# Optimization experiments

Measured on AMD Instinct MI355X. Metric: run time of the kernel, lower is better.

Reference implementation:

```python
import jax, jax.numpy as jnp
from jax import lax
import numpy as np

H, V, B, L, T = 512, 64, 32, 2048, 32


def setup_inputs() -> dict:
    key = jax.random.key(0)
    ks = jax.random.split(key, 24)
    s = 0.05
    n = lambda k, shp: jax.random.normal(k, shp, dtype=jnp.float32) * s
    return {
        "init_decoder_input": jax.random.randint(ks[0], (B,), 0, V),
        "h0": n(ks[1], (1, B, H)),
        "c0": n(ks[2], (1, B, H)),
        "encoder_outputs": jax.random.normal(ks[3], (L, B, H), dtype=jnp.float32),
        "labels": jax.random.randint(ks[4], (T, B), 0, V),
        "mask": jnp.ones((T, B), dtype=bool),
        "target_length": T,
        "embed": n(ks[5], (V, H)),
        "W_ih": n(ks[6], (4 * H, H)),
        "W_hh": n(ks[7], (4 * H, H)),
        "b_ih": n(ks[8], (4 * H,)),
        "b_hh": n(ks[9], (4 * H,)),
        "W_concat": n(ks[10], (H, 2 * H)),
        "b_concat": n(ks[11], (H,)),
        "W_out": n(ks[12], (V, H)),
        "b_out": n(ks[13], (V,)),
        "conv_w": n(ks[14], (H, 1, 3)),
        "conv_b": n(ks[15], (H,)),
        "Wq": n(ks[16], (H, H)),
        "Wv": n(ks[17], (H, H)),
        "Ws": n(ks[18], (1, H)),
        "bs": n(ks[19], (1,)),
        "attn_bias": jax.random.uniform(ks[20], (H,), minval=-0.1, maxval=0.1, dtype=jnp.float32),
    }


def reference(init_decoder_input, h0, c0, encoder_outputs, labels, mask, target_length,
              embed, W_ih, W_hh, b_ih, b_hh, W_concat, b_concat, W_out, b_out,
              conv_w, conv_b, Wq, Wv, Ws, bs, attn_bias):
    value = jnp.transpose(encoder_outputs, (1, 0, 2))        # (B, L, H)
    v_proj = value @ Wv.T                                    # value_proj is step-invariant: hoist out of loop
    bsz = value.shape[0]

    def step(carry, xs):
        h, c, last_attn, dec_in, loss = carry
        lab, msk = xs
        # --- embedding + LSTM cell (torch gate order i,f,g,o) ---
        emb = embed[dec_in]                                  # (B, H)
        gates = emb @ W_ih.T + b_ih + h @ W_hh.T + b_hh
        i, f, g, o = jnp.split(gates, 4, axis=-1)
        c_new = jax.nn.sigmoid(f) * c + jax.nn.sigmoid(i) * jnp.tanh(g)
        h_new = jax.nn.sigmoid(o) * jnp.tanh(c_new)
        # --- location-aware attention ---
        conv_attn = lax.conv_general_dilated(
            last_attn[:, None, :], conv_w, (1,), [(1, 1)],
            dimension_numbers=("NCH", "OIH", "NCH"))         # (B, H, L)
        conv_attn = jnp.transpose(conv_attn, (0, 2, 1)) + conv_b  # (B, L, H)
        q = (h_new @ Wq.T)[:, None, :]                       # (B, 1, H)
        score = jnp.squeeze(jnp.tanh(q + v_proj + conv_attn + attn_bias) @ Ws.T, -1) + bs[0]  # (B, L)
        score = jax.nn.sigmoid(score)                        # smoothing=True
        attn = score / jnp.sum(score, axis=-1, keepdims=True)
        context = jnp.einsum("bl,blh->bh", attn, value)
        # --- concat + output ---
        concat_out = jnp.tanh(jnp.concatenate([h_new, context], axis=-1) @ W_concat.T + b_concat)
        logits = concat_out @ W_out.T + b_out                # (B, V)
        probs = jax.nn.softmax(logits, axis=-1)
        pred = jnp.argmax(probs, axis=-1)                    # greedy feedback (detached)
        # --- masked NLL on softmax probs ---
        ce = -jnp.log(probs[jnp.arange(bsz), lab])
        m = msk.astype(probs.dtype)
        step_loss = jnp.sum(ce * m) / jnp.maximum(jnp.sum(m), 1.0)
        step_loss = jnp.where(jnp.any(msk), step_loss, jnp.zeros((), probs.dtype))
        return (h_new, c_new, attn, pred, loss + step_loss), pred

    carry0 = (h0[0], c0[0], jnp.zeros((bsz, value.shape[1]), value.dtype),
              init_decoder_input, jnp.zeros((), jnp.float32))
    (_, _, _, _, loss), preds = lax.scan(step, carry0, (labels, mask))
    return loss, preds.T                                     # (B, T)
```

## Files before the change

### kernel.cpp

```cpp
#include <hip/hip_runtime.h>
#include <math.h>


#define Hdim 512
#define Vdim 64
#define Bdim 32
#define Ldim 2048
#define Tdim 32
#define CLEN 32
#define NCH 64

__device__ __forceinline__ float sigmoid_f(float x) {
  return 1.0f / (1.0f + __expf(-x));
}
__device__ __forceinline__ float tanh_f(float x) {
  float ax = fabsf(x);
  float e = __expf(2.0f * ax);
  float r = 1.0f - 2.0f / (e + 1.0f);
  return copysignf(r, x);
}

__global__ void k_init(const int* __restrict__ init_in, const float* __restrict__ h0,
                       const float* __restrict__ c0, float* __restrict__ h,
                       float* __restrict__ c, float* __restrict__ Sprev,
                       float* __restrict__ ssum, int* __restrict__ curin,
                       float* __restrict__ lossb) {
  int i = blockIdx.x * blockDim.x + threadIdx.x;
  if (i < Bdim * Hdim) { h[i] = h0[i]; c[i] = c0[i]; }
  if (i < Bdim * Ldim) Sprev[i] = 0.0f;
  if (i < Bdim) { ssum[32 + i] = 1.0f; curin[i] = init_in[i]; }
  if (i == 0) lossb[0] = 0.0f;
}

__global__ void k_pack(const float* __restrict__ conv_w, const float* __restrict__ conv_b,
                       const float* __restrict__ attn_bias, const float* __restrict__ Ws,
                       float4* __restrict__ P4, float* __restrict__ cbab) {
  int h = blockIdx.x * blockDim.x + threadIdx.x;
  if (h < Hdim) {
    P4[h] = make_float4(conv_w[3 * h], conv_w[3 * h + 1], conv_w[3 * h + 2], Ws[h]);
    cbab[h] = conv_b[h] + attn_bias[h];
  }
}

__global__ void k_transpose(const float* __restrict__ in, float* __restrict__ out,
                            int R, int C) {
  int i = blockIdx.x * blockDim.x + threadIdx.x;
  if (i < R * C) { int r = i / C, c = i % C; out[(size_t)c * R + r] = in[i]; }
}

__global__ __launch_bounds__(256) void k_matT16(
    const float* __restrict__ A, const float* __restrict__ W,
    float* __restrict__ out, int Kdim, int Ntot, int mode,
    const int* __restrict__ curin, const float* __restrict__ ex1,
    const float* __restrict__ ex2) {
  __shared__ float a_lds[64][33];
  __shared__ float w_lds[64][17];
  const int tid = threadIdx.x;
  const int n0 = blockIdx.x * 16;
  const int m0 = blockIdx.y * 32;
  const int tm = tid >> 3;
  const int tn = tid & 7;
  float acc0 = 0.f, acc1 = 0.f;
  for (int k0 = 0; k0 < Kdim; k0 += 64) {
    {
      const int m = tid & 31, kg = tid >> 5;
      const float* ap = A + (size_t)(m0 + m) * Kdim + k0 + kg * 8;
      float4 v0 = *(const float4*)ap;
      float4 v1 = *(const float4*)(ap + 4);
      const int kk = kg * 8;
      a_lds[kk + 0][m] = v0.x; a_lds[kk + 1][m] = v0.y;
      a_lds[kk + 2][m] = v0.z; a_lds[kk + 3][m] = v0.w;
      a_lds[kk + 4][m] = v1.x; a_lds[kk + 5][m] = v1.y;
      a_lds[kk + 6][m] = v1.z; a_lds[kk + 7][m] = v1.w;
    }
    if (tid < 128) {
      const int r = tid & 15, kg = tid >> 4;
      const float* wp = W + (size_t)(n0 + r) * Kdim + k0 + kg * 8;
      float4 v0 = *(const float4*)wp;
      float4 v1 = *(const float4*)(wp + 4);
      const int kk = kg * 8;
      w_lds[kk + 0][r] = v0.x; w_lds[kk + 1][r] = v0.y;
      w_lds[kk + 2][r] = v0.z; w_lds[kk + 3][r] = v0.w;
      w_lds[kk + 4][r] = v1.x; w_lds[kk + 5][r] = v1.y;
      w_lds[kk + 6][r] = v1.z; w_lds[kk + 7][r] = v1.w;
    }
    __syncthreads();
#pragma unroll 16
    for (int kk = 0; kk < 64; kk++) {
      const float a = a_lds[kk][tm];
      acc0 += a * w_lds[kk][tn * 2];
      acc1 += a * w_lds[kk][tn * 2 + 1];
    }
    __syncthreads();
  }
  const int gm = m0 + tm;
#pragma unroll
  for (int c = 0; c < 2; c++) {
    const int n = n0 + tn * 2 + c;
    const float a = (c == 0) ? acc0 : acc1;
    float r;
    if (mode == 0)      r = a + ex1[(size_t)curin[gm] * 2048 + n];
    else if (mode == 1) r = a + ex1[n];
    else if (mode == 2) r = a + ex1[n] + ex2[n];
    else                r = tanh_f(a + ex1[n]);
    out[(size_t)gm * Ntot + n] = r;
  }
}

__global__ __launch_bounds__(256) void k_vproj(const float* __restrict__ enc,
                                               const float* __restrict__ Wv,
                                               float* __restrict__ vp) {
  __shared__ float At[8][128];
  __shared__ float Bt[8][128];
  const int tid = threadIdx.x;
  const int r0 = blockIdx.x * 128;
  const int c0 = blockIdx.y * 128;
  const int tx = tid & 15;
  const int ty = tid >> 4;
  float acc[8][8];
#pragma unroll
  for (int i = 0; i < 8; i++)
#pragma unroll
    for (int j = 0; j < 8; j++) acc[i][j] = 0.f;

  for (int k0 = 0; k0 < Hdim; k0 += 8) {
    {
      const int r = tid & 127;
      const int kg = tid >> 7;
      const int gr = r0 + r;
      const int b = gr >> 11;
      const int l = gr & (Ldim - 1);
      const float* ap = enc + ((size_t)l * Bdim + b) * Hdim + k0 + kg * 4;
      float4 v = *(const float4*)ap;
      At[kg * 4 + 0][r] = v.x; At[kg * 4 + 1][r] = v.y;
      At[kg * 4 + 2][r] = v.z; At[kg * 4 + 3][r] = v.w;
      const float* wp = Wv + (size_t)(c0 + r) * Hdim + k0 + kg * 4;
      float4 w = *(const float4*)wp;
      Bt[kg * 4 + 0][r] = w.x; Bt[kg * 4 + 1][r] = w.y;
      Bt[kg * 4 + 2][r] = w.z; Bt[kg * 4 + 3][r] = w.w;
    }
    __syncthreads();
#pragma unroll
    for (int kk = 0; kk < 8; kk++) {
      float a[8], bb[8];
      *(float4*)&a[0] = *(const float4*)&At[kk][ty * 8];
      *(float4*)&a[4] = *(const float4*)&At[kk][ty * 8 + 4];
      *(float4*)&bb[0] = *(const float4*)&Bt[kk][tx * 4];
      *(float4*)&bb[4] = *(const float4*)&Bt[kk][64 + tx * 4];
#pragma unroll
      for (int i = 0; i < 8; i++)
#pragma unroll
        for (int j = 0; j < 8; j++) acc[i][j] += a[i] * bb[j];
    }
    __syncthreads();
  }
#pragma unroll
  for (int i = 0; i < 8; i++) {
    float* orow = vp + (size_t)(r0 + ty * 8 + i) * Hdim + c0;
    float4 o0 = {acc[i][0], acc[i][1], acc[i][2], acc[i][3]};
    float4 o1 = {acc[i][4], acc[i][5], acc[i][6], acc[i][7]};
    *(float4*)(orow + tx * 4) = o0;
    *(float4*)(orow + 64 + tx * 4) = o1;
  }
}

__global__ void k_cell(const float* __restrict__ gates, float* __restrict__ h,
                       float* __restrict__ c, float* __restrict__ ssum_cur) {
  int i = blockIdx.x * blockDim.x + threadIdx.x;
  if (blockIdx.x == 0 && threadIdx.x < Bdim) ssum_cur[threadIdx.x] = 0.f;
  int b = i >> 9, hh = i & 511;
  const float* g = gates + (size_t)b * 2048;
  float gi = g[hh], gf = g[512 + hh], gg = g[1024 + hh], go = g[1536 + hh];
  float cn = sigmoid_f(gf) * c[i] + sigmoid_f(gi) * tanh_f(gg);
  float hn = sigmoid_f(go) * tanh_f(cn);
  c[i] = cn;
  h[i] = hn;
}

__global__ __launch_bounds__(256) void k_sctx(
    const float* __restrict__ vp, const float* __restrict__ q2,
    const float* __restrict__ Sprev, const float* __restrict__ ssum_prev,
    const float4* __restrict__ P4, const float* __restrict__ bs,
    const float* __restrict__ enc, float* __restrict__ Scur,
    float* __restrict__ ssum_cur, float* __restrict__ pctx) {
  __shared__ float pad[4][512];
  __shared__ float wsum[4];
  const int chunk = blockIdx.x & (NCH - 1);
  const int b = blockIdx.x >> 6;
  const int tid = threadIdx.x;
  const int wave = tid >> 6, lane = tid & 63;
  const int l0 = chunk * CLEN + wave * 8;

  float4 pp[8];
#pragma unroll
  for (int e = 0; e < 8; e++) pp[e] = P4[lane * 8 + e];
  float qv[8];
  {
    const float* qrow = q2 + (size_t)b * Hdim + lane * 8;
    *(float4*)&qv[0] = *(const float4*)qrow;
    *(float4*)&qv[4] = *(const float4*)(qrow + 4);
  }
  const float inv = 1.0f / ssum_prev[b];
  const float* sp = Sprev + (size_t)b * Ldim;
  const float bsv = bs[0];

  float acc[8];
#pragma unroll
  for (int e = 0; e < 8; e++) acc[e] = 0.f;
  float csum = 0.f;

#pragma unroll 2
  for (int i = 0; i < 8; i++) {
    const int l = l0 + i;
    const float* vrow = vp + ((size_t)b * Ldim + l) * Hdim + lane * 8;
    const float* erow = enc + ((size_t)l * Bdim + b) * Hdim + lane * 8;
    float vv[8];
    *(float4*)&vv[0] = *(const float4*)vrow;
    *(float4*)&vv[4] = *(const float4*)(vrow + 4);
    const float4 e0 = *(const float4*)erow;
    const float4 e1 = *(const float4*)(erow + 4);
    const float a0 = (l > 0) ? sp[l - 1] * inv : 0.f;
    const float a1 = sp[l] * inv;
    const float a2 = (l < Ldim - 1) ? sp[l + 1] * inv : 0.f;
    float s = 0.f;
#pragma unroll
    for (int e = 0; e < 8; e++) {
      float x = vv[e] + qv[e] + pp[e].x * a0 + pp[e].y * a1 + pp[e].z * a2;
      s += pp[e].w * tanh_f(x);
    }
#pragma unroll
    for (int off = 32; off; off >>= 1) s += __shfl_xor(s, off, 64);
    const float sg = 1.0f / (1.0f + __expf(-(s + bsv)));
    csum += sg;
    if (lane == 0) Scur[(size_t)b * Ldim + l] = sg;
    acc[0] += sg * e0.x; acc[1] += sg * e0.y;
    acc[2] += sg * e0.z; acc[3] += sg * e0.w;
    acc[4] += sg * e1.x; acc[5] += sg * e1.y;
    acc[6] += sg * e1.z; acc[7] += sg * e1.w;
  }
  *(float4*)&pad[wave][lane * 8] = *(float4*)&acc[0];
  *(float4*)&pad[wave][lane * 8 + 4] = *(float4*)&acc[4];
  if (lane == 0) wsum[wave] = csum;
  __syncthreads();
  float* o = pctx + ((size_t)b * NCH + chunk) * Hdim;
  o[tid] = pad[0][tid] + pad[1][tid] + pad[2][tid] + pad[3][tid];
  o[tid + 256] = pad[0][tid + 256] + pad[1][tid + 256] + pad[2][tid + 256] + pad[3][tid + 256];
  if (tid == 0) atomicAdd(ssum_cur + b, wsum[0] + wsum[1] + wsum[2] + wsum[3]);
}

__global__ __launch_bounds__(256) void k_hcat(
    const float* __restrict__ h, const float* __restrict__ pctx,
    const float* __restrict__ ssum, float* __restrict__ hcat) {
  __shared__ float4 red[256];
  const int b = blockIdx.x;
  const int tid = threadIdx.x;
  const float inv = 1.0f / ssum[b];
  const float4* p4 = (const float4*)(pctx + (size_t)b * NCH * Hdim);
  const int q = tid & 127, ch0 = tid >> 7;
  float4 a = {0.f, 0.f, 0.f, 0.f};
  for (int ch = ch0; ch < NCH; ch += 2) {
    float4 v = p4[ch * 128 + q];
    a.x += v.x; a.y += v.y; a.z += v.z; a.w += v.w;
  }
  red[tid] = a;
  hcat[(size_t)b * 1024 + tid] = h[(size_t)b * Hdim + tid];
  hcat[(size_t)b * 1024 + tid + 256] = h[(size_t)b * Hdim + tid + 256];
  __syncthreads();
  if (tid < 128) {
    float4 r0 = red[tid], r1 = red[tid + 128];
    float4 c4 = {(r0.x + r1.x) * inv, (r0.y + r1.y) * inv,
                 (r0.z + r1.z) * inv, (r0.w + r1.w) * inv};
    *(float4*)&hcat[(size_t)b * 1024 + 512 + q * 4] = c4;
  }
}

__global__ __launch_bounds__(256) void k_out2(
    const float* __restrict__ co, const float* __restrict__ WoT,
    const float* __restrict__ b_out, const int* __restrict__ labels, int t,
    int* __restrict__ curin, float* __restrict__ lossb, float* __restrict__ d_out) {
  __shared__ float cs[512];
  const int b = blockIdx.x;
  const int tid = threadIdx.x;
  cs[tid] = co[(size_t)b * Hdim + tid];
  cs[tid + 256] = co[(size_t)b * Hdim + tid + 256];
  __syncthreads();
  if (tid < 64) {
    float l0 = 0.f, l1 = 0.f, l2 = 0.f, l3 = 0.f;
    for (int k = 0; k < 512; k += 4) {
      l0 += cs[k] * WoT[(size_t)k * 64 + tid];
      l1 += cs[k + 1] * WoT[(size_t)(k + 1) * 64 + tid];
      l2 += cs[k + 2] * WoT[(size_t)(k + 2) * 64 + tid];
      l3 += cs[k + 3] * WoT[(size_t)(k + 3) * 64 + tid];
    }
    const float lg = ((l0 + l1) + (l2 + l3)) + b_out[tid];
    float mx = lg;
    int mi = tid;
#pragma unroll
    for (int off = 32; off; off >>= 1) {
      float ov = __shfl_xor(mx, off, 64);
      int oi = __shfl_xor(mi, off, 64);
      if (ov > mx || (ov == mx && oi < mi)) { mx = ov; mi = oi; }
    }
    float se = __expf(lg - mx);
#pragma unroll
    for (int off = 32; off; off >>= 1) se += __shfl_xor(se, off, 64);
    const int lab = labels[t * Bdim + b];
    const float lg_lab = __shfl(lg, lab, 64);
    if (tid == 0) {
      const float ce = -(lg_lab - mx - __logf(se));
      atomicAdd(lossb, ce * (1.0f / 32.0f));
      curin[b] = mi;
      d_out[1 + b * Tdim + t] = (float)mi;
    }
  }
}

__global__ void k_final(const float* __restrict__ lossb, float* __restrict__ d_out) {
  if (threadIdx.x == 0) d_out[0] = lossb[0];
}

extern "C" void kernel_launch(void* const* d_in, const int* in_sizes, int n_in,
                              void* d_out, int out_size, void* d_ws, size_t ws_size,
                              hipStream_t stream) {
  const int* init_in = (const int*)d_in[0];
  const float* h0 = (const float*)d_in[1];
  const float* c0 = (const float*)d_in[2];
  const float* enc = (const float*)d_in[3];
  const int* labels = (const int*)d_in[4];
  const float* embed = (const float*)d_in[7];
  const float* W_ih = (const float*)d_in[8];
  const float* W_hh = (const float*)d_in[9];
  const float* b_ih = (const float*)d_in[10];
  const float* b_hh = (const float*)d_in[11];
  const float* W_concat = (const float*)d_in[12];
  const float* b_concat = (const float*)d_in[13];
  const float* W_out = (const float*)d_in[14];
  const float* b_out = (const float*)d_in[15];
  const float* conv_w = (const float*)d_in[16];
  const float* conv_b = (const float*)d_in[17];
  const float* Wq = (const float*)d_in[18];
  const float* Wv = (const float*)d_in[19];
  const float* Ws_ = (const float*)d_in[20];
  const float* bs = (const float*)d_in[21];
  const float* attn_bias = (const float*)d_in[22];
  float* out = (float*)d_out;

  float* ws = (float*)d_ws;
  size_t off = 0;
  auto alloc = [&](size_t n) {
    float* p = ws + off;
    off += (n + 63) & ~(size_t)63;
    return p;
  };
  float* vp = alloc((size_t)Bdim * Ldim * Hdim);
  float* embW = alloc(Vdim * 2048);
  float* WoT = alloc(512 * 64);
  float* P4b = alloc(512 * 4);
  float* cbab = alloc(512);
  float* gates = alloc(Bdim * 2048);
  float* hA = alloc(Bdim * Hdim);
  float* hB = alloc(Bdim * Hdim);
  float* cbuf = alloc(Bdim * Hdim);
  float* q2 = alloc(Bdim * Hdim);
  float* S0 = alloc(Bdim * Ldim);
  float* S1 = alloc(Bdim * Ldim);
  float* ssum = alloc(64);
  float* pctx = alloc((size_t)Bdim * NCH * Hdim);
  float* hcatb = alloc(Bdim * 1024);
  float* cob = alloc(Bdim * Hdim);
  float* lossb = alloc(64);
  int* curin = (int*)alloc(64);
  (void)ws_size; (void)in_sizes; (void)n_in; (void)out_size;

  k_init<<<256, 256, 0, stream>>>(init_in, h0, c0, hA, cbuf, S1, ssum, curin, lossb);
  k_pack<<<2, 256, 0, stream>>>(conv_w, conv_b, attn_bias, Ws_, (float4*)P4b, cbab);
  k_transpose<<<(64 * 512 + 255) / 256, 256, 0, stream>>>(W_out, WoT, 64, 512);
  k_matT16<<<dim3(128, 2), 256, 0, stream>>>(embed, W_ih, embW, 512, 2048, 2,
                                             nullptr, b_ih, b_hh);
  k_vproj<<<dim3(512, 4), 256, 0, stream>>>(enc, Wv, vp);

  for (int t = 0; t < Tdim; t++) {
    const int cur = t & 1;
    float* Scur = cur ? S1 : S0;
    float* Sprev = cur ? S0 : S1;
    float* hprev = cur ? hB : hA;
    float* hnew = cur ? hA : hB;
    float* ssum_cur = ssum + cur * 32;
    float* ssum_prev = ssum + (cur ^ 1) * 32;
    k_matT16<<<dim3(128, 1), 256, 0, stream>>>(hprev, W_hh, gates, 512, 2048, 0,
                                               curin, embW, nullptr);
    k_cell<<<64, 256, 0, stream>>>(gates, hnew, cbuf, ssum_cur);
    k_matT16<<<dim3(32, 1), 256, 0, stream>>>(hnew, Wq, q2, 512, 512, 1,
                                              nullptr, cbab, nullptr);
    k_sctx<<<Bdim * NCH, 256, 0, stream>>>(vp, q2, Sprev, ssum_prev, (const float4*)P4b,
                                           bs, enc, Scur, ssum_cur, pctx);
    k_hcat<<<32, 256, 0, stream>>>(hnew, pctx, ssum_cur, hcatb);
    k_matT16<<<dim3(32, 1), 256, 0, stream>>>(hcatb, W_concat, cob, 1024, 512, 3,
                                              nullptr, b_concat, nullptr);
    k_out2<<<32, 256, 0, stream>>>(cob, WoT, b_out, labels, t, curin, lossb, out);
  }
  k_final<<<1, 64, 0, stream>>>(lossb, out);
}
```

Before: 5.303 ms.

## Interleave projected values with encoder rows and fuse gate GEMM with LSTM cell

Adds an interleaved buffer that stores v_proj and a batch-major copy of encoder_outputs side by side per (b,l) row, so the attention kernel reads both from one contiguous 4KB row instead of two strided locations. It also fuses the W_hh gate GEMM with the LSTM cell update into one kernel that computes all four gates per output column, which removes the gates round-trip and a launch per step. The cost is a larger workspace and an extra copy pass at setup. There is a fallback to the old layout when the workspace is too small.

New measurement: 6.522 ms. +23.0%, slower.

```diff
diff --git a/kernel.cpp b/kernel.cpp
--- a/kernel.cpp
+++ b/kernel.cpp
@@ -48,11 +48,18 @@
   if (i < R * C) { int r = i / C, c = i % C; out[(size_t)c * R + r] = in[i]; }
 }
 
+__global__ void k_copyenc(const float* __restrict__ enc, float* __restrict__ VE) {
+  const int r = blockIdx.x;
+  const int b = r & (Bdim - 1);
+  const int l = r >> 5;
+  const float4 v = *(const float4*)(enc + (size_t)r * Hdim + threadIdx.x * 4);
+  *(float4*)(VE + ((size_t)b * Ldim + l) * 1024 + 512 + threadIdx.x * 4) = v;
+}
+
 __global__ __launch_bounds__(256) void k_matT16(
     const float* __restrict__ A, const float* __restrict__ W,
     float* __restrict__ out, int Kdim, int Ntot, int mode,
-    const int* __restrict__ curin, const float* __restrict__ ex1,
-    const float* __restrict__ ex2) {
+    const float* __restrict__ ex1, const float* __restrict__ ex2) {
   __shared__ float a_lds[64][33];
   __shared__ float w_lds[64][17];
   const int tid = threadIdx.x;
@@ -99,8 +106,7 @@
     const int n = n0 + tn * 2 + c;
     const float a = (c == 0) ? acc0 : acc1;
     float r;
-    if (mode == 0)      r = a + ex1[(size_t)curin[gm] * 2048 + n];
-    else if (mode == 1) r = a + ex1[n];
+    if (mode == 1)      r = a + ex1[n];
     else if (mode == 2) r = a + ex1[n] + ex2[n];
     else                r = tanh_f(a + ex1[n]);
     out[(size_t)gm * Ntot + n] = r;
@@ -109,7 +115,7 @@
 
 __global__ __launch_bounds__(256) void k_vproj(const float* __restrict__ enc,
                                                const float* __restrict__ Wv,
-                                               float* __restrict__ vp) {
+                                               float* __restrict__ vp, int ostride) {
   __shared__ float At[8][128];
   __shared__ float Bt[8][128];
   const int tid = threadIdx.x;
@@ -156,7 +162,7 @@
   }
 #pragma unroll
   for (int i = 0; i < 8; i++) {
-    float* orow = vp + (size_t)(r0 + ty * 8 + i) * Hdim + c0;
+    float* orow = vp + (size_t)(r0 + ty * 8 + i) * ostride + c0;
     float4 o0 = {acc[i][0], acc[i][1], acc[i][2], acc[i][3]};
     float4 o1 = {acc[i][4], acc[i][5], acc[i][6], acc[i][7]};
     *(float4*)(orow + tx * 4) = o0;
@@ -164,25 +170,72 @@
   }
 }
 
-__global__ void k_cell(const float* __restrict__ gates, float* __restrict__ h,
-                       float* __restrict__ c, float* __restrict__ ssum_cur) {
-  int i = blockIdx.x * blockDim.x + threadIdx.x;
-  if (blockIdx.x == 0 && threadIdx.x < Bdim) ssum_cur[threadIdx.x] = 0.f;
-  int b = i >> 9, hh = i & 511;
-  const float* g = gates + (size_t)b * 2048;
-  float gi = g[hh], gf = g[512 + hh], gg = g[1024 + hh], go = g[1536 + hh];
-  float cn = sigmoid_f(gf) * c[i] + sigmoid_f(gi) * tanh_f(gg);
-  float hn = sigmoid_f(go) * tanh_f(cn);
-  c[i] = cn;
-  h[i] = hn;
+__global__ __launch_bounds__(256) void k_gatecell(
+    const float* __restrict__ hprev, const float* __restrict__ W_hh,
+    const float* __restrict__ embW, const int* __restrict__ curin,
+    float* __restrict__ hnew, float* __restrict__ cbuf,
+    float* __restrict__ ssum_zero) {
+  __shared__ float a_lds[32][68];
+  __shared__ float w_lds[4][16][68];
+  const int tid = threadIdx.x;
+  const int n0 = blockIdx.x * 16;
+  if (blockIdx.x == 0 && tid < Bdim) ssum_zero[tid] = 0.f;
+  const int tm = tid >> 3;
+  const int tn = tid & 7;
+  float acc[4][2] = {};
+  for (int k0 = 0; k0 < Hdim; k0 += 64) {
+    {
+      const int m = tid & 31, kg = tid >> 5;
+      const float* ap = hprev + (size_t)m * Hdim + k0 + kg * 8;
+      float4 v0 = *(const float4*)ap, v1 = *(const float4*)(ap + 4);
+      *(float4*)&a_lds[m][kg * 8] = v0;
+      *(float4*)&a_lds[m][kg * 8 + 4] = v1;
+    }
+    {
+      const int g = tid >> 6, r = (tid >> 2) & 15, kq = tid & 3;
+      const float* wp = W_hh + (size_t)(g * Hdim + n0 + r) * Hdim + k0 + kq * 16;
+#pragma unroll
+      for (int q = 0; q < 4; q++) {
+        float4 v = *(const float4*)(wp + q * 4);
+        *(float4*)&w_lds[g][r][kq * 16 + q * 4] = v;
+      }
+    }
+    __syncthreads();
+#pragma unroll
+    for (int kk = 0; kk < 64; kk += 4) {
+      float4 a4 = *(const float4*)&a_lds[tm][kk];
+#pragma unroll
+      for (int g = 0; g < 4; g++) {
+        float4 w0 = *(const float4*)&w_lds[g][tn * 2][kk];
+        float4 w1 = *(const float4*)&w_lds[g][tn * 2 + 1][kk];
+        acc[g][0] += a4.x * w0.x + a4.y * w0.y + a4.z * w0.z + a4.w * w0.w;
+        acc[g][1] += a4.x * w1.x + a4.y * w1.y + a4.z * w1.z + a4.w * w1.w;
+      }
+    }
+    __syncthreads();
+  }
+  const int m = tm;
+  const float* ew = embW + (size_t)curin[m] * 2048;
+#pragma unroll
+  for (int c = 0; c < 2; c++) {
+    const int n = n0 + tn * 2 + c;
+    const float gi = acc[0][c] + ew[n];
+    const float gf = acc[1][c] + ew[512 + n];
+    const float gg = acc[2][c] + ew[1024 + n];
+    const float go = acc[3][c] + ew[1536 + n];
+    const float cn = sigmoid_f(gf) * cbuf[(size_t)m * Hdim + n] + sigmoid_f(gi) * tanh_f(gg);
+    const float hn = sigmoid_f(go) * tanh_f(cn);
+    cbuf[(size_t)m * Hdim + n] = cn;
+    hnew[(size_t)m * Hdim + n] = hn;
+  }
 }
 
 __global__ __launch_bounds__(256) void k_sctx(
-    const float* __restrict__ vp, const float* __restrict__ q2,
-    const float* __restrict__ Sprev, const float* __restrict__ ssum_prev,
-    const float4* __restrict__ P4, const float* __restrict__ bs,
-    const float* __restrict__ enc, float* __restrict__ Scur,
-    float* __restrict__ ssum_cur, float* __restrict__ pctx) {
+    const float* __restrict__ vbase, const float* __restrict__ ebase,
+    const float* __restrict__ q2, const float* __restrict__ Sprev,
+    const float* __restrict__ ssum_prev, const float4* __restrict__ P4,
+    const float* __restrict__ bs, float* __restrict__ Scur,
+    float* __restrict__ ssum_cur, float* __restrict__ pctx, int mode) {
   __shared__ float pad[4][512];
   __shared__ float wsum[4];
   const int chunk = blockIdx.x & (NCH - 1);
@@ -212,8 +265,15 @@
 #pragma unroll 2
   for (int i = 0; i < 8; i++) {
     const int l = l0 + i;
-    const float* vrow = vp + ((size_t)b * Ldim + l) * Hdim + lane * 8;
-    const float* erow = enc + ((size_t)l * Bdim + b) * Hdim + lane * 8;
+    const float* vrow;
+    const float* erow;
+    if (mode) {
+      vrow = vbase + ((size_t)b * Ldim + l) * 1024 + lane * 8;
+      erow = vrow + 512;
+    } else {
+      vrow = vbase + ((size_t)b * Ldim + l) * 512 + lane * 8;
+      erow = ebase + ((size_t)l * Bdim + b) * 512 + lane * 8;
+    }
     float vv[8];
     *(float4*)&vv[0] = *(const float4*)vrow;
     *(float4*)&vv[4] = *(const float4*)(vrow + 4);
@@ -345,6 +405,10 @@
   const float* attn_bias = (const float*)d_in[22];
   float* out = (float*)d_out;
 
+  const size_t ve_floats = (size_t)Bdim * Ldim * 1024;
+  const size_t tail_floats = 4u * 1024 * 1024;
+  const bool useVE = ws_size >= (ve_floats + tail_floats) * sizeof(float);
+
   float* ws = (float*)d_ws;
   size_t off = 0;
   auto alloc = [&](size_t n) {
@@ -352,12 +416,11 @@
     off += (n + 63) & ~(size_t)63;
     return p;
   };
-  float* vp = alloc((size_t)Bdim * Ldim * Hdim);
+  float* big = alloc(useVE ? ve_floats : (size_t)Bdim * Ldim * Hdim);
   float* embW = alloc(Vdim * 2048);
   float* WoT = alloc(512 * 64);
   float* P4b = alloc(512 * 4);
   float* cbab = alloc(512);
-  float* gates = alloc(Bdim * 2048);
   float* hA = alloc(Bdim * Hdim);
   float* hB = alloc(Bdim * Hdim);
   float* cbuf = alloc(Bdim * Hdim);
@@ -370,14 +433,15 @@
   float* cob = alloc(Bdim * Hdim);
   float* lossb = alloc(64);
   int* curin = (int*)alloc(64);
-  (void)ws_size; (void)in_sizes; (void)n_in; (void)out_size;
+  (void)in_sizes; (void)n_in; (void)out_size;
 
   k_init<<<256, 256, 0, stream>>>(init_in, h0, c0, hA, cbuf, S1, ssum, curin, lossb);
   k_pack<<<2, 256, 0, stream>>>(conv_w, conv_b, attn_bias, Ws_, (float4*)P4b, cbab);
   k_transpose<<<(64 * 512 + 255) / 256, 256, 0, stream>>>(W_out, WoT, 64, 512);
   k_matT16<<<dim3(128, 2), 256, 0, stream>>>(embed, W_ih, embW, 512, 2048, 2,
-                                             nullptr, b_ih, b_hh);
-  k_vproj<<<dim3(512, 4), 256, 0, stream>>>(enc, Wv, vp);
+                                             b_ih, b_hh);
+  k_vproj<<<dim3(512, 4), 256, 0, stream>>>(enc, Wv, big, useVE ? 1024 : 512);
+  if (useVE) k_copyenc<<<Bdim * Ldim, 128, 0, stream>>>(enc, big);
 
   for (int t = 0; t < Tdim; t++) {
     const int cur = t & 1;
@@ -387,16 +451,15 @@
     float* hnew = cur ? hA : hB;
     float* ssum_cur = ssum + cur * 32;
     float* ssum_prev = ssum + (cur ^ 1) * 32;
-    k_matT16<<<dim3(128, 1), 256, 0, stream>>>(hprev, W_hh, gates, 512, 2048, 0,
-                                               curin, embW, nullptr);
-    k_cell<<<64, 256, 0, stream>>>(gates, hnew, cbuf, ssum_cur);
+    k_gatecell<<<32, 256, 0, stream>>>(hprev, W_hh, embW, curin, hnew, cbuf, ssum_cur);
     k_matT16<<<dim3(32, 1), 256, 0, stream>>>(hnew, Wq, q2, 512, 512, 1,
-                                              nullptr, cbab, nullptr);
-    k_sctx<<<Bdim * NCH, 256, 0, stream>>>(vp, q2, Sprev, ssum_prev, (const float4*)P4b,
-                                           bs, enc, Scur, ssum_cur, pctx);
+                                              cbab, nullptr);
+    k_sctx<<<Bdim * NCH, 256, 0, stream>>>(big, enc, q2, Sprev, ssum_prev,
+                                           (const float4*)P4b, bs, Scur, ssum_cur,
+                                           pctx, useVE ? 1 : 0);
     k_hcat<<<32, 256, 0, stream>>>(hnew, pctx, ssum_cur, hcatb);
     k_matT16<<<dim3(32, 1), 256, 0, stream>>>(hcatb, W_concat, cob, 1024, 512, 3,
-                                              nullptr, b_concat, nullptr);
+                                              b_concat, nullptr);
     k_out2<<<32, 256, 0, stream>>>(cob, WoT, b_out, labels, t, curin, lossb, out);
   }
   k_final<<<1, 64, 0, stream>>>(lossb, out);
```

## Fuse context reduction, concat projection and output head into one kernel

Applied to the files above, without the earlier changes.

Merges k_hcat, the W_concat matmul and k_out2 into a single per-batch k_head kernel. The hcat and concat_out buffers now live in shared memory, and W_concat is pre-transposed once so that each block computes all 512 concat outputs. This removes two launches per step and their global round-trips. In exchange, each of only 32 blocks now streams the full 2MB W_concat, so this stage has far less parallelism than the previous 32-block matT16 tiling across outputs.

After: 4.967 ms. -6.3%, faster.

```diff
diff --git a/kernel.cpp b/kernel.cpp
--- a/kernel.cpp
+++ b/kernel.cpp
@@ -248,49 +248,56 @@
   if (tid == 0) atomicAdd(ssum_cur + b, wsum[0] + wsum[1] + wsum[2] + wsum[3]);
 }
 
-__global__ __launch_bounds__(256) void k_hcat(
+__global__ __launch_bounds__(256) void k_head(
     const float* __restrict__ h, const float* __restrict__ pctx,
-    const float* __restrict__ ssum, float* __restrict__ hcat) {
-  __shared__ float4 red[256];
+    const float* __restrict__ ssum, const float* __restrict__ WcT,
+    const float* __restrict__ b_concat, const float* __restrict__ WoT,
+    const float* __restrict__ b_out, const int* __restrict__ labels, int t,
+    int* __restrict__ curin, float* __restrict__ lossb, float* __restrict__ d_out) {
+  __shared__ float hcat[1024];
+  __shared__ float part[2][512];
+  __shared__ float co[512];
   const int b = blockIdx.x;
   const int tid = threadIdx.x;
   const float inv = 1.0f / ssum[b];
-  const float4* p4 = (const float4*)(pctx + (size_t)b * NCH * Hdim);
-  const int q = tid & 127, ch0 = tid >> 7;
-  float4 a = {0.f, 0.f, 0.f, 0.f};
-  for (int ch = ch0; ch < NCH; ch += 2) {
-    float4 v = p4[ch * 128 + q];
-    a.x += v.x; a.y += v.y; a.z += v.z; a.w += v.w;
-  }
-  red[tid] = a;
-  hcat[(size_t)b * 1024 + tid] = h[(size_t)b * Hdim + tid];
-  hcat[(size_t)b * 1024 + tid + 256] = h[(size_t)b * Hdim + tid + 256];
+  {
+    float c0 = 0.f, c1 = 0.f;
+    const float* p = pctx + (size_t)b * NCH * Hdim;
+#pragma unroll 8
+    for (int ch = 0; ch < NCH; ch++) {
+      c0 += p[(size_t)ch * Hdim + tid];
+      c1 += p[(size_t)ch * Hdim + tid + 256];
+    }
+    hcat[tid] = h[(size_t)b * Hdim + tid];
+    hcat[tid + 256] = h[(size_t)b * Hdim + tid + 256];
+    hcat[512 + tid] = c0 * inv;
+    hcat[512 + tid + 256] = c1 * inv;
+  }
   __syncthreads();
-  if (tid < 128) {
-    float4 r0 = red[tid], r1 = red[tid + 128];
-    float4 c4 = {(r0.x + r1.x) * inv, (r0.y + r1.y) * inv,
-                 (r0.z + r1.z) * inv, (r0.w + r1.w) * inv};
-    *(float4*)&hcat[(size_t)b * 1024 + 512 + q * 4] = c4;
-  }
-}
-
-__global__ __launch_bounds__(256) void k_out2(
-    const float* __restrict__ co, const float* __restrict__ WoT,
-    const float* __restrict__ b_out, const int* __restrict__ labels, int t,
-    int* __restrict__ curin, float* __restrict__ lossb, float* __restrict__ d_out) {
-  __shared__ float cs[512];
-  const int b = blockIdx.x;
-  const int tid = threadIdx.x;
-  cs[tid] = co[(size_t)b * Hdim + tid];
-  cs[tid + 256] = co[(size_t)b * Hdim + tid + 256];
+  {
+    const int half = tid >> 7;
+    const int c4 = (tid & 127) * 4;
+    float4 a4 = {0.f, 0.f, 0.f, 0.f};
+    const float* wbase = WcT + (size_t)half * 512 * 512 + c4;
+    const float* hb = &hcat[half * 512];
+    for (int k = 0; k < 512; k++) {
+      const float a = hb[k];
+      const float4 w = *(const float4*)(wbase + (size_t)k * 512);
+      a4.x += a * w.x; a4.y += a * w.y; a4.z += a * w.z; a4.w += a * w.w;
+    }
+    *(float4*)&part[half][c4] = a4;
+  }
+  __syncthreads();
+  co[tid] = tanh_f(part[0][tid] + part[1][tid] + b_concat[tid]);
+  co[tid + 256] = tanh_f(part[0][tid + 256] + part[1][tid + 256] + b_concat[tid + 256]);
   __syncthreads();
   if (tid < 64) {
     float l0 = 0.f, l1 = 0.f, l2 = 0.f, l3 = 0.f;
     for (int k = 0; k < 512; k += 4) {
-      l0 += cs[k] * WoT[(size_t)k * 64 + tid];
-      l1 += cs[k + 1] * WoT[(size_t)(k + 1) * 64 + tid];
-      l2 += cs[k + 2] * WoT[(size_t)(k + 2) * 64 + tid];
-      l3 += cs[k + 3] * WoT[(size_t)(k + 3) * 64 + tid];
+      l0 += co[k] * WoT[(size_t)k * 64 + tid];
+      l1 += co[k + 1] * WoT[(size_t)(k + 1) * 64 + tid];
+      l2 += co[k + 2] * WoT[(size_t)(k + 2) * 64 + tid];
+      l3 += co[k + 3] * WoT[(size_t)(k + 3) * 64 + tid];
     }
     const float lg = ((l0 + l1) + (l2 + l3)) + b_out[tid];
     float mx = lg;
@@ -355,6 +362,7 @@
   float* vp = alloc((size_t)Bdim * Ldim * Hdim);
   float* embW = alloc(Vdim * 2048);
   float* WoT = alloc(512 * 64);
+  float* WcT = alloc(1024 * 512);
   float* P4b = alloc(512 * 4);
   float* cbab = alloc(512);
   float* gates = alloc(Bdim * 2048);
@@ -366,8 +374,6 @@
   float* S1 = alloc(Bdim * Ldim);
   float* ssum = alloc(64);
   float* pctx = alloc((size_t)Bdim * NCH * Hdim);
-  float* hcatb = alloc(Bdim * 1024);
-  float* cob = alloc(Bdim * Hdim);
   float* lossb = alloc(64);
   int* curin = (int*)alloc(64);
   (void)ws_size; (void)in_sizes; (void)n_in; (void)out_size;
@@ -375,6 +381,7 @@
   k_init<<<256, 256, 0, stream>>>(init_in, h0, c0, hA, cbuf, S1, ssum, curin, lossb);
   k_pack<<<2, 256, 0, stream>>>(conv_w, conv_b, attn_bias, Ws_, (float4*)P4b, cbab);
   k_transpose<<<(64 * 512 + 255) / 256, 256, 0, stream>>>(W_out, WoT, 64, 512);
+  k_transpose<<<(512 * 1024 + 255) / 256, 256, 0, stream>>>(W_concat, WcT, 512, 1024);
   k_matT16<<<dim3(128, 2), 256, 0, stream>>>(embed, W_ih, embW, 512, 2048, 2,
                                              nullptr, b_ih, b_hh);
   k_vproj<<<dim3(512, 4), 256, 0, stream>>>(enc, Wv, vp);
@@ -394,10 +401,8 @@
                                               nullptr, cbab, nullptr);
     k_sctx<<<Bdim * NCH, 256, 0, stream>>>(vp, q2, Sprev, ssum_prev, (const float4*)P4b,
                                            bs, enc, Scur, ssum_cur, pctx);
-    k_hcat<<<32, 256, 0, stream>>>(hnew, pctx, ssum_cur, hcatb);
-    k_matT16<<<dim3(32, 1), 256, 0, stream>>>(hcatb, W_concat, cob, 1024, 512, 3,
-                                              nullptr, b_concat, nullptr);
-    k_out2<<<32, 256, 0, stream>>>(cob, WoT, b_out, labels, t, curin, lossb, out);
+    k_head<<<32, 256, 0, stream>>>(hnew, pctx, ssum_cur, WcT, b_concat, WoT, b_out,
+                                   labels, t, curin, lossb, out);
   }
   k_final<<<1, 64, 0, stream>>>(lossb, out);
 }
```
